# Performance work log

Measured on AMD Instinct MI355X. Metric: run time of the kernel, lower is better.

Reference implementation:

```python
import jax, jax.numpy as jnp
import numpy as np

V, E, H = 50257, 256, 256
B, S = 64, 2048


def setup_inputs() -> dict:
    key = jax.random.key(0)
    ks = jax.random.split(key, 24)
    u = (1.0 / H) ** 0.5
    def U(k, shape):
        return jax.random.uniform(k, shape, jnp.float32, -u, u)
    inp = {
        "inputs": jax.random.randint(ks[0], (B, S), 0, V, dtype=jnp.int32),
        "h0": jax.random.normal(ks[1], (1, B, H), jnp.float32),
        "c0": jax.random.normal(ks[2], (1, B, H), jnp.float32),
        "emb": jax.random.normal(ks[3], (V, E), jnp.float32) * 0.02,
    }
    for i, n in enumerate(["w_ii", "w_if", "w_ig", "w_io"]):
        inp[n] = U(ks[4 + i], (H, E))
    for i, n in enumerate(["w_hi", "w_hf", "w_hg", "w_ho"]):
        inp[n] = U(ks[8 + i], (H, H))
    for i, n in enumerate(["b_ii", "b_if", "b_ig", "b_io", "b_hi", "b_hf", "b_hg", "b_ho"]):
        inp[n] = U(ks[12 + i], (H,))
    return inp


def _lstm(x, h0, c0, w_ii, w_if, w_ig, w_io, w_hi, w_hf, w_hg, w_ho,
          b_ii, b_if, b_ig, b_io, b_hi, b_hf, b_hg, b_ho):
    # x: (B, S, E). Precompute all input projections (batched GEMMs) once.
    xi = jnp.einsum('bse,he->bsh', x, w_ii) + b_ii + b_hi  # (B,S,H)
    xf = jnp.einsum('bse,he->bsh', x, w_if) + b_if + b_hf
    xg = jnp.einsum('bse,he->bsh', x, w_ig) + b_ig + b_hg
    xo = jnp.einsum('bse,he->bsh', x, w_io) + b_io + b_ho
    # move time to leading axis for scan: (S,B,H)
    xs = (xi.transpose(1, 0, 2), xf.transpose(1, 0, 2),
          xg.transpose(1, 0, 2), xo.transpose(1, 0, 2))

    def step(carry, ts):
        h, c = carry  # (B,H)
        xi_t, xf_t, xg_t, xo_t = ts
        i_t = jax.nn.sigmoid(xi_t + h @ w_hi.T)
        f_t = jax.nn.sigmoid(xf_t + h @ w_hf.T)
        g_t = jnp.tanh(xg_t + h @ w_hg.T)
        o_t = jax.nn.sigmoid(xo_t + h @ w_ho.T)
        c_new = f_t * c + i_t * g_t
        h_new = o_t * jnp.tanh(c_new)
        return (h_new, c_new), h_new

    (h_f, c_f), out = jax.lax.scan(step, (h0[0], c0[0]), xs)  # out: (S,B,H)
    return out.transpose(1, 0, 2), h_f[None], c_f[None]


def reference(inputs, h0, c0, emb, w_ii, w_if, w_ig, w_io, w_hi, w_hf, w_hg, w_ho,
              b_ii, b_if, b_ig, b_io, b_hi, b_hf, b_hg, b_ho):
    # nn.Embedding(padding_idx=0): row 0 is zero and receives no gradient
    emb_z = emb.at[0].set(0.0)
    x = emb_z[inputs]  # (B,S,E)
    return _lstm(x, h0, c0, w_ii, w_if, w_ig, w_io, w_hi, w_hf, w_hg, w_ho,
                 b_ii, b_if, b_ig, b_io, b_hi, b_hf, b_hg, b_ho)
```

## Files before the change

### kernel.cpp

```cpp
#include <hip/hip_runtime.h>
#include <hip/hip_fp16.h>
#include <cstdint>
#include <cstddef>

#define B_ 64
#define S_ 2048
#define H_ 256
#define E_ 256
#define NG 1024

typedef __attribute__((ext_vector_type(8))) short short8v;
typedef __attribute__((ext_vector_type(4))) float float4v;
typedef __fp16 half2v __attribute__((ext_vector_type(2)));

__device__ __forceinline__ short f2bf(float f) {
  uint32_t u = __float_as_uint(f);
  u = (u + 0x7fffu + ((u >> 16) & 1u)) >> 16;
  return (short)u;
}
__device__ __forceinline__ float sigf(float x) { return 1.f / (1.f + __expf(-x)); }
__device__ __forceinline__ float tanhf_fast(float x) {
  float ax = fabsf(x);
  float e = __expf(-2.f * ax);
  float t = (1.f - e) / (1.f + e);
  return copysignf(t, x);
}
__device__ __forceinline__ uint32_t pkh2(float a, float b) {
  return __builtin_bit_cast(uint32_t, __floats2half2_rn(a, b));
}

__device__ __forceinline__ float dot2f(uint32_t w, uint32_t h, float acc) {
#if __has_builtin(__builtin_amdgcn_fdot2)
  return __builtin_amdgcn_fdot2(__builtin_bit_cast(half2v, w),
                                __builtin_bit_cast(half2v, h), acc, false);
#else
  __half2 hw = __builtin_bit_cast(__half2, w);
  __half2 hh = __builtin_bit_cast(__half2, h);
  acc = fmaf(__half2float(hw.x), __half2float(hh.x), acc);
  acc = fmaf(__half2float(hw.y), __half2float(hh.y), acc);
  return acc;
#endif
}

__device__ __forceinline__ float red_q4(float x) {
  x += __builtin_bit_cast(float, __builtin_amdgcn_update_dpp(
           0, __builtin_bit_cast(int, x), 0x128, 0xf, 0xf, true));
  float a = x, b = x;
  asm("v_permlane32_swap_b32 %0, %1" : "+v"(a), "+v"(b));
  return a + b;
}

#define SYNC_LDS() asm volatile("s_waitcnt lgkmcnt(0)\n\ts_barrier" ::: "memory")

__global__ __launch_bounds__(256, 2)
void lstm_xproj(const int* __restrict__ idx, const float* __restrict__ emb,
                const float* __restrict__ w0, const float* __restrict__ w1,
                const float* __restrict__ w2, const float* __restrict__ w3,
                const float* __restrict__ bi0, const float* __restrict__ bi1,
                const float* __restrict__ bi2, const float* __restrict__ bi3,
                const float* __restrict__ bh0, const float* __restrict__ bh1,
                const float* __restrict__ bh2, const float* __restrict__ bh3,
                __half* __restrict__ pre, int s0, int Cc) {
  __shared__ __align__(16) short Ak[4][128][8];
  __shared__ __align__(16) short Bk[4][128][8];
  __shared__ int ridx[128];

  const int tid = threadIdx.x;
  const int bm = blockIdx.x, bn = blockIdx.y;
  const int n0 = bn * 128;
  const int g = bn >> 1;
  const int ng = (bn & 1) * 128;
  const float* wp  = (g == 0) ? w0  : (g == 1) ? w1  : (g == 2) ? w2  : w3;
  const float* bip = (g == 0) ? bi0 : (g == 1) ? bi1 : (g == 2) ? bi2 : bi3;
  const float* bhp = (g == 0) ? bh0 : (g == 1) ? bh1 : (g == 2) ? bh2 : bh3;

  if (tid < 128) {
    int m = bm * 128 + tid;
    int bb = m / Cc;
    int ss = m - bb * Cc;
    ridx[tid] = idx[bb * S_ + s0 + ss];
  }

  float4v z = {0.f, 0.f, 0.f, 0.f};
  float4v acc[4][4];
#pragma unroll
  for (int mi = 0; mi < 4; ++mi)
#pragma unroll
    for (int ni = 0; ni < 4; ++ni) acc[mi][ni] = z;

  const int wv = tid >> 6, lane = tid & 63;
  const int wr = wv >> 1, wc = wv & 1;
  const int lr = lane & 15, ks = lane >> 4;
  const int sr = tid >> 3, seg = tid & 7;

  for (int kt = 0; kt < 8; ++kt) {
    const int k0 = kt * 32;
    __syncthreads();
#pragma unroll
    for (int it = 0; it < 4; ++it) {
      int r = sr + it * 32;
      int tok = ridx[r];
      float4 va = make_float4(0.f, 0.f, 0.f, 0.f);
      if (tok != 0) va = *(const float4*)(emb + (size_t)tok * E_ + k0 + seg * 4);
      short4 sa; sa.x = f2bf(va.x); sa.y = f2bf(va.y); sa.z = f2bf(va.z); sa.w = f2bf(va.w);
      *(short4*)&Ak[seg >> 1][r][(seg & 1) * 4] = sa;
      float4 vb = *(const float4*)(wp + (size_t)(ng + r) * E_ + k0 + seg * 4);
      short4 sb; sb.x = f2bf(vb.x); sb.y = f2bf(vb.y); sb.z = f2bf(vb.z); sb.w = f2bf(vb.w);
      *(short4*)&Bk[seg >> 1][r][(seg & 1) * 4] = sb;
    }
    __syncthreads();
    short8v af[4], bfv[4];
#pragma unroll
    for (int mi = 0; mi < 4; ++mi) af[mi] = *(short8v*)&Ak[ks][wr * 64 + mi * 16 + lr][0];
#pragma unroll
    for (int ni = 0; ni < 4; ++ni) bfv[ni] = *(short8v*)&Bk[ks][wc * 64 + ni * 16 + lr][0];
#pragma unroll
    for (int mi = 0; mi < 4; ++mi)
#pragma unroll
      for (int ni = 0; ni < 4; ++ni)
        acc[mi][ni] = __builtin_amdgcn_mfma_f32_16x16x32_bf16(af[mi], bfv[ni], acc[mi][ni], 0, 0, 0);
  }

#pragma unroll
  for (int ni = 0; ni < 4; ++ni) {
    int jj = ng + wc * 64 + ni * 16 + lr;
    float bias = bip[jj] + bhp[jj];
    int jglob = n0 + wc * 64 + ni * 16 + lr;
#pragma unroll
    for (int mi = 0; mi < 4; ++mi) {
#pragma unroll
      for (int rr = 0; rr < 4; ++rr) {
        int m = bm * 128 + wr * 64 + mi * 16 + (lane >> 4) * 4 + rr;
        pre[(size_t)m * NG + jglob] = __float2half(acc[mi][ni][rr] + bias);
      }
    }
  }
}

__global__ __launch_bounds__(512, 2)
void lstm_rec(const __half* __restrict__ pre,
              const float* wh_i, const float* wh_f,
              const float* wh_g, const float* wh_o,
              const float* __restrict__ h0, const float* __restrict__ c0,
              float* out, float* cstate,
              int s0, int Cc) {
  __shared__ uint32_t wlds32[256 * 128];
  __shared__ uint32_t hshp[288];

  const int b = blockIdx.x;
  const int t = threadIdx.x;
  const int lane = t & 63, wave = t >> 6;
  const int q4 = ((lane >> 3) & 1) | ((lane >> 5) << 1);
  const int jp = (wave << 4) | (((lane >> 4) & 1) << 3) | (lane & 7);
  const int j0 = 2 * jp;
  const bool fin = ((lane & 40) == 0);
  const int sw = (jp & 7) << 2;

#pragma unroll 8
  for (int i = 0; i < 64; ++i) {
    int idx2 = t + 512 * i;
    int row = idx2 >> 7, col = idx2 & 127;
    float2 v = *(const float2*)(wh_o + 2 * idx2);
    wlds32[row * 128 + (col ^ (((row >> 1) & 7) << 2))] = pkh2(v.x, v.y);
  }

  uint32_t wI0[32], wI1[32], wF0[32], wF1[32], wG0[32], wG1[32];
  {
    const float4* pI0 = (const float4*)(wh_i + (size_t)j0 * 256 + q4 * 64);
    const float4* pI1 = (const float4*)(wh_i + (size_t)(j0 + 1) * 256 + q4 * 64);
    const float4* pF0 = (const float4*)(wh_f + (size_t)j0 * 256 + q4 * 64);
    const float4* pF1 = (const float4*)(wh_f + (size_t)(j0 + 1) * 256 + q4 * 64);
    const float4* pG0 = (const float4*)(wh_g + (size_t)j0 * 256 + q4 * 64);
    const float4* pG1 = (const float4*)(wh_g + (size_t)(j0 + 1) * 256 + q4 * 64);
#pragma unroll
    for (int k = 0; k < 16; ++k) {
      float4 v;
      v = pI0[k]; wI0[2 * k] = pkh2(v.x, v.y); wI0[2 * k + 1] = pkh2(v.z, v.w);
      v = pI1[k]; wI1[2 * k] = pkh2(v.x, v.y); wI1[2 * k + 1] = pkh2(v.z, v.w);
      v = pF0[k]; wF0[2 * k] = pkh2(v.x, v.y); wF0[2 * k + 1] = pkh2(v.z, v.w);
      v = pF1[k]; wF1[2 * k] = pkh2(v.x, v.y); wF1[2 * k + 1] = pkh2(v.z, v.w);
      v = pG0[k]; wG0[2 * k] = pkh2(v.x, v.y); wG0[2 * k + 1] = pkh2(v.z, v.w);
      v = pG1[k]; wG1[2 * k] = pkh2(v.x, v.y); wG1[2 * k + 1] = pkh2(v.z, v.w);
    }
  }

  if (t < 128) {
    float2 hp = (s0 == 0) ? *(const float2*)(h0 + b * H_ + 2 * t)
                          : *(const float2*)(cstate + b * 512 + 256 + 2 * t);
    hshp[(t >> 5) * 36 + (t & 31)] = pkh2(hp.x, hp.y);
  }
  float cR0 = 0.f, cR1 = 0.f, hN0 = 0.f, hN1 = 0.f;
  if (fin) {
    float2 cv = (s0 == 0) ? *(const float2*)(c0 + b * H_ + j0)
                          : *(const float2*)(cstate + b * 512 + j0);
    cR0 = cv.x; cR1 = cv.y;
  }
  __syncthreads();

  const uint32_t* pb32 = (const uint32_t*)(pre + (size_t)b * (size_t)Cc * NG);
  const uint32_t* wrow0 = wlds32 + (size_t)j0 * 128 + q4 * 32;
  const uint32_t* wrow1 = wrow0 + 128;
  const uint32_t* hqA = hshp + q4 * 36;
  const uint32_t* hqB = hqA + 144;
  uint32_t* hwB = hshp + (jp >> 5) * 36 + (jp & 31);
  uint32_t* hwA = hwB + 144;
  float* outp = out + ((size_t)b * S_ + s0) * H_ + j0;

#define HV_(c8)  (*(const uint4*)(hq + (c8) * 4))
#define WO0_(c8) (*(const uint4*)(wrow0 + (((c8) * 4) ^ sw)))
#define WO1_(c8) (*(const uint4*)(wrow1 + (((c8) * 4) ^ sw)))
#define CONS_(c8, hv, wa, wb)                                   \
  aO0 = dot2f(wa.x, hv.x, aO0); aO0 = dot2f(wa.y, hv.y, aO0);   \
  aO0 = dot2f(wa.z, hv.z, aO0); aO0 = dot2f(wa.w, hv.w, aO0);   \
  aO1 = dot2f(wb.x, hv.x, aO1); aO1 = dot2f(wb.y, hv.y, aO1);   \
  aO1 = dot2f(wb.z, hv.z, aO1); aO1 = dot2f(wb.w, hv.w, aO1);   \
  aI0 = dot2f(wI0[(c8) * 4 + 0], hv.x, aI0);                    \
  aI0 = dot2f(wI0[(c8) * 4 + 1], hv.y, aI0);                    \
  aI0 = dot2f(wI0[(c8) * 4 + 2], hv.z, aI0);                    \
  aI0 = dot2f(wI0[(c8) * 4 + 3], hv.w, aI0);                    \
  aI1 = dot2f(wI1[(c8) * 4 + 0], hv.x, aI1);                    \
  aI1 = dot2f(wI1[(c8) * 4 + 1], hv.y, aI1);                    \
  aI1 = dot2f(wI1[(c8) * 4 + 2], hv.z, aI1);                    \
  aI1 = dot2f(wI1[(c8) * 4 + 3], hv.w, aI1);                    \
  aF0 = dot2f(wF0[(c8) * 4 + 0], hv.x, aF0);                    \
  aF0 = dot2f(wF0[(c8) * 4 + 1], hv.y, aF0);                    \
  aF0 = dot2f(wF0[(c8) * 4 + 2], hv.z, aF0);                    \
  aF0 = dot2f(wF0[(c8) * 4 + 3], hv.w, aF0);                    \
  aF1 = dot2f(wF1[(c8) * 4 + 0], hv.x, aF1);                    \
  aF1 = dot2f(wF1[(c8) * 4 + 1], hv.y, aF1);                    \
  aF1 = dot2f(wF1[(c8) * 4 + 2], hv.z, aF1);                    \
  aF1 = dot2f(wF1[(c8) * 4 + 3], hv.w, aF1);                    \
  aG0 = dot2f(wG0[(c8) * 4 + 0], hv.x, aG0);                    \
  aG0 = dot2f(wG0[(c8) * 4 + 1], hv.y, aG0);                    \
  aG0 = dot2f(wG0[(c8) * 4 + 2], hv.z, aG0);                    \
  aG0 = dot2f(wG0[(c8) * 4 + 3], hv.w, aG0);                    \
  aG1 = dot2f(wG1[(c8) * 4 + 0], hv.x, aG1);                    \
  aG1 = dot2f(wG1[(c8) * 4 + 1], hv.y, aG1);                    \
  aG1 = dot2f(wG1[(c8) * 4 + 2], hv.z, aG1);                    \
  aG1 = dot2f(wG1[(c8) * 4 + 3], hv.w, aG1);

#define BODY_(HQ, HW)                                                       \
  {                                                                         \
    uint32_t pC0 = 0, pC1 = 0, pC2 = 0, pC3 = 0;                            \
    if (fin) {                                                              \
      const uint32_t* pp = pb32 + (size_t)tl * 512;                         \
      pC0 = pp[jp];       pC1 = pp[128 + jp];                               \
      pC2 = pp[256 + jp]; pC3 = pp[384 + jp];                               \
    }                                                                       \
    const uint32_t* hq = (HQ);                                              \
    float aI0 = 0.f, aI1 = 0.f, aF0 = 0.f, aF1 = 0.f;                       \
    float aG0 = 0.f, aG1 = 0.f, aO0 = 0.f, aO1 = 0.f;                       \
    {                                                                       \
      uint4 hvA = HV_(0), hvB = HV_(1), hvC = HV_(2);                       \
      CONS_(0, hvA, waA, wbA);                                              \
      waA = WO0_(2); wbA = WO1_(2); hvA = HV_(3);                           \
      CONS_(1, hvB, waB, wbB);                                              \
      waB = WO0_(3); wbB = WO1_(3); hvB = HV_(4);                           \
      CONS_(2, hvC, waA, wbA);                                              \
      waA = WO0_(4); wbA = WO1_(4); hvC = HV_(5);                           \
      CONS_(3, hvA, waB, wbB);                                              \
      waB = WO0_(5); wbB = WO1_(5); hvA = HV_(6);                           \
      CONS_(4, hvB, waA, wbA);                                              \
      waA = WO0_(6); wbA = WO1_(6); hvB = HV_(7);                           \
      CONS_(5, hvC, waB, wbB);                                              \
      waB = WO0_(7); wbB = WO1_(7);                                         \
      CONS_(6, hvA, waA, wbA);                                              \
      waA = WO0_(0); wbA = WO1_(0);                \
      CONS_(7, hvB, waB, wbB);                                              \
      waB = WO0_(1); wbB = WO1_(1);                \
    }                                                                       \
    aI0 = red_q4(aI0); aI1 = red_q4(aI1);                                   \
    aF0 = red_q4(aF0); aF1 = red_q4(aF1);                                   \
    aG0 = red_q4(aG0); aG1 = red_q4(aG1);                                   \
    aO0 = red_q4(aO0); aO1 = red_q4(aO1);                                   \
    if (fin) {                                                              \
      float2 pI = __half22float2(__builtin_bit_cast(__half2, pC0));         \
      float2 pF = __half22float2(__builtin_bit_cast(__half2, pC1));         \
      float2 pG = __half22float2(__builtin_bit_cast(__half2, pC2));         \
      float2 pO = __half22float2(__builtin_bit_cast(__half2, pC3));         \
      float xi0 = aI0 + pI.x, xi1 = aI1 + pI.y;                             \
      float xf0 = aF0 + pF.x, xf1 = aF1 + pF.y;                             \
      float xg0 = aG0 + pG.x, xg1 = aG1 + pG.y;                             \
      float xo0 = aO0 + pO.x, xo1 = aO1 + pO.y;                             \
      cR0 = sigf(xf0) * cR0 + sigf(xi0) * tanhf_fast(xg0);                  \
      cR1 = sigf(xf1) * cR1 + sigf(xi1) * tanhf_fast(xg1);                  \
      hN0 = sigf(xo0) * tanhf_fast(cR0);                                    \
      hN1 = sigf(xo1) * tanhf_fast(cR1);                                    \
      *(float2*)outp = make_float2(hN0, hN1);                               \
      *(HW) = pkh2(hN0, hN1);                                               \
    }                                                                       \
    outp += H_;                                                             \
    ++tl;                                                                   \
    SYNC_LDS();                                                             \
  }

  uint4 waA = WO0_(0), wbA = WO1_(0);
  uint4 waB = WO0_(1), wbB = WO1_(1);

  int tl = 0;
  while (tl < Cc) {
    BODY_(hqA, hwA);
    BODY_(hqB, hwB);
  }
#undef BODY_
#undef CONS_
#undef WO1_
#undef WO0_
#undef HV_

  if (fin) {
    *(float2*)(cstate + b * 512 + j0) = make_float2(cR0, cR1);
    *(float2*)(cstate + b * 512 + 256 + j0) = make_float2(hN0, hN1);
    if (s0 + Cc == S_) {
      float* hfp = out + (size_t)B_ * S_ * H_;
      float* cfp = hfp + (size_t)B_ * H_;
      *(float2*)(hfp + b * H_ + j0) = make_float2(hN0, hN1);
      *(float2*)(cfp + b * H_ + j0) = make_float2(cR0, cR1);
    }
  }
}

extern "C" void kernel_launch(void* const* d_in, const int* in_sizes, int n_in,
                              void* d_out, int out_size, void* d_ws, size_t ws_size,
                              hipStream_t stream) {
  (void)in_sizes; (void)n_in; (void)out_size;
  const int* idx = (const int*)d_in[0];
  const float* h0 = (const float*)d_in[1];
  const float* c0 = (const float*)d_in[2];
  const float* emb = (const float*)d_in[3];
  const float* w_ii = (const float*)d_in[4];
  const float* w_if = (const float*)d_in[5];
  const float* w_ig = (const float*)d_in[6];
  const float* w_io = (const float*)d_in[7];
  const float* w_hi = (const float*)d_in[8];
  const float* w_hf = (const float*)d_in[9];
  const float* w_hg = (const float*)d_in[10];
  const float* w_ho = (const float*)d_in[11];
  const float* b_ii = (const float*)d_in[12];
  const float* b_if = (const float*)d_in[13];
  const float* b_ig = (const float*)d_in[14];
  const float* b_io = (const float*)d_in[15];
  const float* b_hi = (const float*)d_in[16];
  const float* b_hf = (const float*)d_in[17];
  const float* b_hg = (const float*)d_in[18];
  const float* b_ho = (const float*)d_in[19];
  float* out = (float*)d_out;

  char* ws = (char*)d_ws;
  float* cstate = (float*)ws;
  __half* pre = (__half*)(ws + 131072);
  size_t avail = (ws_size > 131072) ? ws_size - 131072 : 0;
  long long cmax = (long long)(avail / ((size_t)B_ * NG * sizeof(__half)));
  int C = (int)((cmax > S_) ? S_ : cmax);
  C &= ~1;
  if (C < 2) C = 2;

  for (int s0 = 0; s0 < S_; s0 += C) {
    int Cc = (S_ - s0 < C) ? (S_ - s0) : C;
    dim3 gg((unsigned)((64 * Cc) / 128), 8);
    lstm_xproj<<<gg, 256, 0, stream>>>(idx, emb, w_ii, w_if, w_ig, w_io,
                                       b_ii, b_if, b_ig, b_io,
                                       b_hi, b_hf, b_hg, b_ho, pre, s0, Cc);
    lstm_rec<<<64, 512, 0, stream>>>(pre, w_hi, w_hf, w_hg, w_ho, h0, c0,
                                     out, cstate, s0, Cc);
  }
}
```

Measured before the change: 4.122 ms.

## Use 1024-thread recurrent blocks with one hidden unit per thread

The recurrent kernel now launches 1024 threads per batch row and gives each thread-group a single hidden unit instead of a pair. This halves per-thread register weights and dot-product work per timestep, which shortens the serial critical path of each step. In exchange there are twice as many waves to synchronize per step, h is written to shared memory as 16-bit halves, and the launch bound of 1024 threads may force register spilling of the 96 per-thread weight registers.

```diff
diff --git a/kernel.cpp b/kernel.cpp
--- a/kernel.cpp
+++ b/kernel.cpp
@@ -137,7 +137,7 @@
   }
 }
 
-__global__ __launch_bounds__(512, 2)
+__global__ __launch_bounds__(1024, 4)
 void lstm_rec(const __half* __restrict__ pre,
               const float* wh_i, const float* wh_f,
               const float* wh_g, const float* wh_o,
@@ -151,36 +151,29 @@
   const int t = threadIdx.x;
   const int lane = t & 63, wave = t >> 6;
   const int q4 = ((lane >> 3) & 1) | ((lane >> 5) << 1);
-  const int jp = (wave << 4) | (((lane >> 4) & 1) << 3) | (lane & 7);
-  const int j0 = 2 * jp;
+  const int j = (wave << 4) | (((lane >> 4) & 1) << 3) | (lane & 7);
   const bool fin = ((lane & 40) == 0);
-  const int sw = (jp & 7) << 2;
+  const int sw = (j & 7) << 2;
 
 #pragma unroll 8
-  for (int i = 0; i < 64; ++i) {
-    int idx2 = t + 512 * i;
-    int row = idx2 >> 7, col = idx2 & 127;
-    float2 v = *(const float2*)(wh_o + 2 * idx2);
-    wlds32[row * 128 + (col ^ (((row >> 1) & 7) << 2))] = pkh2(v.x, v.y);
-  }
-
-  uint32_t wI0[32], wI1[32], wF0[32], wF1[32], wG0[32], wG1[32];
+  for (int i = 0; i < 32; ++i) {
+    int d = t + 1024 * i;
+    int row = d >> 7, col = d & 127;
+    float2 v = *(const float2*)(wh_o + 2 * (size_t)d);
+    wlds32[row * 128 + (col ^ ((row & 7) << 2))] = pkh2(v.x, v.y);
+  }
+
+  uint32_t wI[32], wF[32], wG[32];
   {
-    const float4* pI0 = (const float4*)(wh_i + (size_t)j0 * 256 + q4 * 64);
-    const float4* pI1 = (const float4*)(wh_i + (size_t)(j0 + 1) * 256 + q4 * 64);
-    const float4* pF0 = (const float4*)(wh_f + (size_t)j0 * 256 + q4 * 64);
-    const float4* pF1 = (const float4*)(wh_f + (size_t)(j0 + 1) * 256 + q4 * 64);
-    const float4* pG0 = (const float4*)(wh_g + (size_t)j0 * 256 + q4 * 64);
-    const float4* pG1 = (const float4*)(wh_g + (size_t)(j0 + 1) * 256 + q4 * 64);
+    const float4* pI = (const float4*)(wh_i + (size_t)j * 256 + q4 * 64);
+    const float4* pF = (const float4*)(wh_f + (size_t)j * 256 + q4 * 64);
+    const float4* pG = (const float4*)(wh_g + (size_t)j * 256 + q4 * 64);
 #pragma unroll
     for (int k = 0; k < 16; ++k) {
       float4 v;
-      v = pI0[k]; wI0[2 * k] = pkh2(v.x, v.y); wI0[2 * k + 1] = pkh2(v.z, v.w);
-      v = pI1[k]; wI1[2 * k] = pkh2(v.x, v.y); wI1[2 * k + 1] = pkh2(v.z, v.w);
-      v = pF0[k]; wF0[2 * k] = pkh2(v.x, v.y); wF0[2 * k + 1] = pkh2(v.z, v.w);
-      v = pF1[k]; wF1[2 * k] = pkh2(v.x, v.y); wF1[2 * k + 1] = pkh2(v.z, v.w);
-      v = pG0[k]; wG0[2 * k] = pkh2(v.x, v.y); wG0[2 * k + 1] = pkh2(v.z, v.w);
-      v = pG1[k]; wG1[2 * k] = pkh2(v.x, v.y); wG1[2 * k + 1] = pkh2(v.z, v.w);
+      v = pI[k]; wI[2 * k] = pkh2(v.x, v.y); wI[2 * k + 1] = pkh2(v.z, v.w);
+      v = pF[k]; wF[2 * k] = pkh2(v.x, v.y); wF[2 * k + 1] = pkh2(v.z, v.w);
+      v = pG[k]; wG[2 * k] = pkh2(v.x, v.y); wG[2 * k + 1] = pkh2(v.z, v.w);
     }
   }
 
@@ -189,133 +182,94 @@
                           : *(const float2*)(cstate + b * 512 + 256 + 2 * t);
     hshp[(t >> 5) * 36 + (t & 31)] = pkh2(hp.x, hp.y);
   }
-  float cR0 = 0.f, cR1 = 0.f, hN0 = 0.f, hN1 = 0.f;
-  if (fin) {
-    float2 cv = (s0 == 0) ? *(const float2*)(c0 + b * H_ + j0)
-                          : *(const float2*)(cstate + b * 512 + j0);
-    cR0 = cv.x; cR1 = cv.y;
-  }
+  float cR = 0.f, hN = 0.f;
+  if (fin) cR = (s0 == 0) ? c0[b * H_ + j] : cstate[b * 512 + j];
   __syncthreads();
 
-  const uint32_t* pb32 = (const uint32_t*)(pre + (size_t)b * (size_t)Cc * NG);
-  const uint32_t* wrow0 = wlds32 + (size_t)j0 * 128 + q4 * 32;
-  const uint32_t* wrow1 = wrow0 + 128;
+  const __half* pb16 = pre + (size_t)b * (size_t)Cc * NG;
+  const uint32_t* wrow = wlds32 + (size_t)j * 128 + q4 * 32;
   const uint32_t* hqA = hshp + q4 * 36;
   const uint32_t* hqB = hqA + 144;
-  uint32_t* hwB = hshp + (jp >> 5) * 36 + (jp & 31);
-  uint32_t* hwA = hwB + 144;
-  float* outp = out + ((size_t)b * S_ + s0) * H_ + j0;
+  const int jp = j >> 1;
+  uint16_t* hwB = (uint16_t*)(hshp + (jp >> 5) * 36 + (jp & 31)) + (j & 1);
+  uint16_t* hwA = hwB + 288;
+  float* outp = out + ((size_t)b * S_ + s0) * H_ + j;
 
 #define HV_(c8)  (*(const uint4*)(hq + (c8) * 4))
-#define WO0_(c8) (*(const uint4*)(wrow0 + (((c8) * 4) ^ sw)))
-#define WO1_(c8) (*(const uint4*)(wrow1 + (((c8) * 4) ^ sw)))
-#define CONS_(c8, hv, wa, wb)                                   \
-  aO0 = dot2f(wa.x, hv.x, aO0); aO0 = dot2f(wa.y, hv.y, aO0);   \
-  aO0 = dot2f(wa.z, hv.z, aO0); aO0 = dot2f(wa.w, hv.w, aO0);   \
-  aO1 = dot2f(wb.x, hv.x, aO1); aO1 = dot2f(wb.y, hv.y, aO1);   \
-  aO1 = dot2f(wb.z, hv.z, aO1); aO1 = dot2f(wb.w, hv.w, aO1);   \
-  aI0 = dot2f(wI0[(c8) * 4 + 0], hv.x, aI0);                    \
-  aI0 = dot2f(wI0[(c8) * 4 + 1], hv.y, aI0);                    \
-  aI0 = dot2f(wI0[(c8) * 4 + 2], hv.z, aI0);                    \
-  aI0 = dot2f(wI0[(c8) * 4 + 3], hv.w, aI0);                    \
-  aI1 = dot2f(wI1[(c8) * 4 + 0], hv.x, aI1);                    \
-  aI1 = dot2f(wI1[(c8) * 4 + 1], hv.y, aI1);                    \
-  aI1 = dot2f(wI1[(c8) * 4 + 2], hv.z, aI1);                    \
-  aI1 = dot2f(wI1[(c8) * 4 + 3], hv.w, aI1);                    \
-  aF0 = dot2f(wF0[(c8) * 4 + 0], hv.x, aF0);                    \
-  aF0 = dot2f(wF0[(c8) * 4 + 1], hv.y, aF0);                    \
-  aF0 = dot2f(wF0[(c8) * 4 + 2], hv.z, aF0);                    \
-  aF0 = dot2f(wF0[(c8) * 4 + 3], hv.w, aF0);                    \
-  aF1 = dot2f(wF1[(c8) * 4 + 0], hv.x, aF1);                    \
-  aF1 = dot2f(wF1[(c8) * 4 + 1], hv.y, aF1);                    \
-  aF1 = dot2f(wF1[(c8) * 4 + 2], hv.z, aF1);                    \
-  aF1 = dot2f(wF1[(c8) * 4 + 3], hv.w, aF1);                    \
-  aG0 = dot2f(wG0[(c8) * 4 + 0], hv.x, aG0);                    \
-  aG0 = dot2f(wG0[(c8) * 4 + 1], hv.y, aG0);                    \
-  aG0 = dot2f(wG0[(c8) * 4 + 2], hv.z, aG0);                    \
-  aG0 = dot2f(wG0[(c8) * 4 + 3], hv.w, aG0);                    \
-  aG1 = dot2f(wG1[(c8) * 4 + 0], hv.x, aG1);                    \
-  aG1 = dot2f(wG1[(c8) * 4 + 1], hv.y, aG1);                    \
-  aG1 = dot2f(wG1[(c8) * 4 + 2], hv.z, aG1);                    \
-  aG1 = dot2f(wG1[(c8) * 4 + 3], hv.w, aG1);
+#define WO_(c8)  (*(const uint4*)(wrow + (((c8) * 4) ^ sw)))
+#define STG_(c8, hv, wa)                                        \
+  aO = dot2f(wa.x, hv.x, aO); aO = dot2f(wa.y, hv.y, aO);       \
+  aO = dot2f(wa.z, hv.z, aO); aO = dot2f(wa.w, hv.w, aO);       \
+  aI = dot2f(wI[(c8) * 4 + 0], hv.x, aI);                       \
+  aI = dot2f(wI[(c8) * 4 + 1], hv.y, aI);                       \
+  aI = dot2f(wI[(c8) * 4 + 2], hv.z, aI);                       \
+  aI = dot2f(wI[(c8) * 4 + 3], hv.w, aI);                       \
+  aF = dot2f(wF[(c8) * 4 + 0], hv.x, aF);                       \
+  aF = dot2f(wF[(c8) * 4 + 1], hv.y, aF);                       \
+  aF = dot2f(wF[(c8) * 4 + 2], hv.z, aF);                       \
+  aF = dot2f(wF[(c8) * 4 + 3], hv.w, aF);                       \
+  aG = dot2f(wG[(c8) * 4 + 0], hv.x, aG);                       \
+  aG = dot2f(wG[(c8) * 4 + 1], hv.y, aG);                       \
+  aG = dot2f(wG[(c8) * 4 + 2], hv.z, aG);                       \
+  aG = dot2f(wG[(c8) * 4 + 3], hv.w, aG);
 
 #define BODY_(HQ, HW)                                                       \
   {                                                                         \
-    uint32_t pC0 = 0, pC1 = 0, pC2 = 0, pC3 = 0;                            \
+    float pIv = 0.f, pFv = 0.f, pGv = 0.f, pOv = 0.f;                       \
     if (fin) {                                                              \
-      const uint32_t* pp = pb32 + (size_t)tl * 512;                         \
-      pC0 = pp[jp];       pC1 = pp[128 + jp];                               \
-      pC2 = pp[256 + jp]; pC3 = pp[384 + jp];                               \
+      const __half* pp = pb16 + (size_t)tl * NG + j;                        \
+      pIv = __half2float(pp[0]);                                            \
+      pFv = __half2float(pp[256]);                                          \
+      pGv = __half2float(pp[512]);                                          \
+      pOv = __half2float(pp[768]);                                          \
     }                                                                       \
     const uint32_t* hq = (HQ);                                              \
-    float aI0 = 0.f, aI1 = 0.f, aF0 = 0.f, aF1 = 0.f;                       \
-    float aG0 = 0.f, aG1 = 0.f, aO0 = 0.f, aO1 = 0.f;                       \
+    float aI = 0.f, aF = 0.f, aG = 0.f, aO = 0.f;                           \
     {                                                                       \
-      uint4 hvA = HV_(0), hvB = HV_(1), hvC = HV_(2);                       \
-      CONS_(0, hvA, waA, wbA);                                              \
-      waA = WO0_(2); wbA = WO1_(2); hvA = HV_(3);                           \
-      CONS_(1, hvB, waB, wbB);                                              \
-      waB = WO0_(3); wbB = WO1_(3); hvB = HV_(4);                           \
-      CONS_(2, hvC, waA, wbA);                                              \
-      waA = WO0_(4); wbA = WO1_(4); hvC = HV_(5);                           \
-      CONS_(3, hvA, waB, wbB);                                              \
-      waB = WO0_(5); wbB = WO1_(5); hvA = HV_(6);                           \
-      CONS_(4, hvB, waA, wbA);                                              \
-      waA = WO0_(6); wbA = WO1_(6); hvB = HV_(7);                           \
-      CONS_(5, hvC, waB, wbB);                                              \
-      waB = WO0_(7); wbB = WO1_(7);                                         \
-      CONS_(6, hvA, waA, wbA);                                              \
-      waA = WO0_(0); wbA = WO1_(0);                \
-      CONS_(7, hvB, waB, wbB);                                              \
-      waB = WO0_(1); wbB = WO1_(1);                \
+      uint4 hvA = HV_(0), waA = WO_(0);                                     \
+      uint4 hvB = HV_(1), waB = WO_(1);                                     \
+      STG_(0, hvA, waA); hvA = HV_(2); waA = WO_(2);                        \
+      STG_(1, hvB, waB); hvB = HV_(3); waB = WO_(3);                        \
+      STG_(2, hvA, waA); hvA = HV_(4); waA = WO_(4);                        \
+      STG_(3, hvB, waB); hvB = HV_(5); waB = WO_(5);                        \
+      STG_(4, hvA, waA); hvA = HV_(6); waA = WO_(6);                        \
+      STG_(5, hvB, waB); hvB = HV_(7); waB = WO_(7);                        \
+      STG_(6, hvA, waA);                                                    \
+      STG_(7, hvB, waB);                                                    \
     }                                                                       \
-    aI0 = red_q4(aI0); aI1 = red_q4(aI1);                                   \
-    aF0 = red_q4(aF0); aF1 = red_q4(aF1);                                   \
-    aG0 = red_q4(aG0); aG1 = red_q4(aG1);                                   \
-    aO0 = red_q4(aO0); aO1 = red_q4(aO1);                                   \
+    aI = red_q4(aI); aF = red_q4(aF);                                       \
+    aG = red_q4(aG); aO = red_q4(aO);                                       \
     if (fin) {                                                              \
-      float2 pI = __half22float2(__builtin_bit_cast(__half2, pC0));         \
-      float2 pF = __half22float2(__builtin_bit_cast(__half2, pC1));         \
-      float2 pG = __half22float2(__builtin_bit_cast(__half2, pC2));         \
-      float2 pO = __half22float2(__builtin_bit_cast(__half2, pC3));         \
-      float xi0 = aI0 + pI.x, xi1 = aI1 + pI.y;                             \
-      float xf0 = aF0 + pF.x, xf1 = aF1 + pF.y;                             \
-      float xg0 = aG0 + pG.x, xg1 = aG1 + pG.y;                             \
-      float xo0 = aO0 + pO.x, xo1 = aO1 + pO.y;                             \
-      cR0 = sigf(xf0) * cR0 + sigf(xi0) * tanhf_fast(xg0);                  \
-      cR1 = sigf(xf1) * cR1 + sigf(xi1) * tanhf_fast(xg1);                  \
-      hN0 = sigf(xo0) * tanhf_fast(cR0);                                    \
-      hN1 = sigf(xo1) * tanhf_fast(cR1);                                    \
-      *(float2*)outp = make_float2(hN0, hN1);                               \
-      *(HW) = pkh2(hN0, hN1);                                               \
+      float xi = aI + pIv, xf = aF + pFv;                                   \
+      float xg = aG + pGv, xo = aO + pOv;                                   \
+      cR = sigf(xf) * cR + sigf(xi) * tanhf_fast(xg);                       \
+      hN = sigf(xo) * tanhf_fast(cR);                                       \
+      *outp = hN;                                                           \
+      *(HW) = (uint16_t)(pkh2(hN, 0.f) & 0xffffu);                          \
     }                                                                       \
     outp += H_;                                                             \
     ++tl;                                                                   \
     SYNC_LDS();                                                             \
   }
 
-  uint4 waA = WO0_(0), wbA = WO1_(0);
-  uint4 waB = WO0_(1), wbB = WO1_(1);
-
   int tl = 0;
   while (tl < Cc) {
     BODY_(hqA, hwA);
     BODY_(hqB, hwB);
   }
 #undef BODY_
-#undef CONS_
-#undef WO1_
-#undef WO0_
+#undef STG_
+#undef WO_
 #undef HV_
 
   if (fin) {
-    *(float2*)(cstate + b * 512 + j0) = make_float2(cR0, cR1);
-    *(float2*)(cstate + b * 512 + 256 + j0) = make_float2(hN0, hN1);
+    cstate[b * 512 + j] = cR;
+    cstate[b * 512 + 256 + j] = hN;
     if (s0 + Cc == S_) {
       float* hfp = out + (size_t)B_ * S_ * H_;
       float* cfp = hfp + (size_t)B_ * H_;
-      *(float2*)(hfp + b * H_ + j0) = make_float2(hN0, hN1);
-      *(float2*)(cfp + b * H_ + j0) = make_float2(cR0, cR1);
+      hfp[b * H_ + j] = hN;
+      cfp[b * H_ + j] = cR;
     }
   }
 }
@@ -361,7 +315,7 @@
     lstm_xproj<<<gg, 256, 0, stream>>>(idx, emb, w_ii, w_if, w_ig, w_io,
                                        b_ii, b_if, b_ig, b_io,
                                        b_hi, b_hf, b_hg, b_ho, pre, s0, Cc);
-    lstm_rec<<<64, 512, 0, stream>>>(pre, w_hi, w_hf, w_hg, w_ho, h0, c0,
-                                     out, cstate, s0, Cc);
-  }
-}
+    lstm_rec<<<64, 1024, 0, stream>>>(pre, w_hi, w_hf, w_hg, w_ho, h0, c0,
+                                      out, cstate, s0, Cc);
+  }
+}
```

New measurement: 5.335 ms. +29.4%, slower.
